# Kernel tuning notes

Hardware: AMD Instinct MI355X
Metric: run time of the kernel (lower is better)

## Reference

```python
import jax, jax.numpy as jnp
import numpy as np

N_NODES = 50000
N_REL = 3
N_EDGES = 500000
D_IN, D_HID, D_OUT = 128, 256, 128


def setup_inputs() -> dict:
    key = jax.random.key(0)
    ks = jax.random.split(key, 9)
    def w(k, shape, fan_in):
        return jax.random.normal(k, shape, dtype=jnp.float32) / np.sqrt(fan_in)
    return {
        "x": jax.random.normal(ks[0], (N_NODES, D_IN), dtype=jnp.float32),
        "src": jax.random.randint(ks[1], (N_REL, N_EDGES), 0, N_NODES, dtype=jnp.int32),
        "dst": jax.random.randint(ks[2], (N_REL, N_EDGES), 0, N_NODES, dtype=jnp.int32),
        "w_self1": w(ks[3], (N_REL, D_IN, D_HID), D_IN),
        "w_neigh1": w(ks[4], (N_REL, D_IN, D_HID), D_IN),
        "b1": jnp.zeros((N_REL, D_HID), dtype=jnp.float32),
        "w_self2": w(ks[5], (N_REL, D_HID, D_OUT), D_HID),
        "w_neigh2": w(ks[6], (N_REL, D_HID, D_OUT), D_HID),
        "b2": jnp.zeros((N_REL, D_OUT), dtype=jnp.float32),
    }


def _sage_hetero_layer(x, src, dst, w_self, w_neigh, b):
    """Multi-relation SAGEConv (mean agg); relation outputs summed (HeteroGraphConv default).
    x: [N, din]; src/dst: [R, E]; w_*: [R, din, dout]; b: [R, dout]."""
    n = x.shape[0]

    def per_rel(s, d, ws, wn, bb):
        gathered = jnp.take(x, s, axis=0)                      # [E, din] neighbor gather
        summed = jax.ops.segment_sum(gathered, d, num_segments=n)  # [N, din]
        deg = jax.ops.segment_sum(jnp.ones(s.shape, jnp.float32), d, num_segments=n)
        h_neigh = summed / jnp.maximum(deg, 1.0)[:, None]      # mean, 0 for isolated dst
        return x @ ws + h_neigh @ wn + bb                      # fc_self + fc_neigh + bias

    per_rel_out = jax.vmap(per_rel)(src, dst, w_self, w_neigh, b)  # [R, N, dout]
    return per_rel_out.sum(axis=0)


def reference(x, src, dst, w_self1, w_neigh1, b1, w_self2, w_neigh2, b2):
    h = _sage_hetero_layer(x, src, dst, w_self1, w_neigh1, b1)
    h = jax.nn.relu(h)  # SAGEConv activation in hidden layers
    out = _sage_hetero_layer(h, src, dst, w_self2, w_neigh2, b2)  # last layer: no activation
    return out
```

## Files before the change

kernel.cpp:

```cpp
#include <hip/hip_runtime.h>

#define NN 50000
#define NREL 3
#define NE 500000
#define DIN 128
#define DHID 256
#define DOUT 128

#define NBUK 98
#define CAP 8192
#define EPB 4096
#define NCHK ((NE + EPB - 1) / EPB)
#define PA_BLKS (NREL * NCHK)
#define F2B_BLKS 6250
#define ZROW ((uint)NN << 8)

typedef unsigned int uint;
typedef unsigned short ushort;
typedef __attribute__((ext_vector_type(8))) short bf16x8;
typedef __attribute__((ext_vector_type(4))) float f32x4;
typedef __attribute__((ext_vector_type(2))) float f32x2;

using gptr_t = const __attribute__((address_space(1))) unsigned int*;
using lptr_t = __attribute__((address_space(3))) unsigned int*;

__device__ __forceinline__ ushort f2bf(float f) {
    uint u = __float_as_uint(f);
    uint r = (u + 0x7fffu + ((u >> 16) & 1u)) >> 16;
    return (ushort)r;
}
__device__ __forceinline__ void acc2(f32x2& a, uint u) {
    f32x2 t;
    t.x = __uint_as_float(u << 16);
    t.y = __uint_as_float(u & 0xffff0000u);
    a += t;
}
__device__ __forceinline__ void acc16(f32x2* a, uint4 v) {
    acc2(a[0], v.x); acc2(a[1], v.y); acc2(a[2], v.z); acc2(a[3], v.w);
}

__global__ __launch_bounds__(256) void pass_a_prep(
    const int* __restrict__ src, const int* __restrict__ dst,
    int* __restrict__ bcursor, uint* __restrict__ pairs,
    const float* __restrict__ x, ushort* __restrict__ xb,
    const float* __restrict__ ws1, const float* __restrict__ wn1, ushort* __restrict__ Bt1,
    const float* __restrict__ ws2, const float* __restrict__ wn2, ushort* __restrict__ Bt2,
    const float* __restrict__ b1, float* __restrict__ bsum1,
    const float* __restrict__ b2, float* __restrict__ bsum2,
    ushort* __restrict__ agg0, ushort* __restrict__ agg1, ushort* __restrict__ agg2) {
    int blk = blockIdx.x, tid = threadIdx.x;
    if (blk < PA_BLKS) {
        int r = blk / NCHK;
        int chunk = blk % NCHK;
        int e0 = chunk * EPB;
        int nedge = min(EPB, NE - e0);
        const int* S = src + (size_t)r * NE + e0;
        const int* D = dst + (size_t)r * NE + e0;
        __shared__ int cnt[NBUK], base[NBUK], cur[NBUK];
        if (tid < NBUK) { cnt[tid] = 0; cur[tid] = 0; }
        __syncthreads();
        uint pk[16];
        int bk[16];
        bool val[16];
#pragma unroll
        for (int j = 0; j < 16; ++j) {
            int e = j * 256 + tid;
            val[j] = e < nedge;
            int d = val[j] ? D[e] : 0;
            int s = val[j] ? S[e] : 0;
            bk[j] = d >> 9;
            pk[j] = ((uint)s << 9) | (uint)(d & 511);
            if (val[j]) atomicAdd(&cnt[bk[j]], 1);
        }
        __syncthreads();
        if (tid < NBUK) base[tid] = atomicAdd(&bcursor[r * NBUK + tid], cnt[tid]);
        __syncthreads();
#pragma unroll
        for (int j = 0; j < 16; ++j) {
            if (val[j]) {
                int slot = base[bk[j]] + atomicAdd(&cur[bk[j]], 1);
                if (slot < CAP) pairs[(size_t)(r * NBUK + bk[j]) * CAP + slot] = pk[j];
            }
        }
        return;
    }
    blk -= PA_BLKS;
    if (blk < F2B_BLKS) {
        int t = blk * 256 + tid;
        float4 v = *(const float4*)(x + (size_t)t * 4);
        uint2 p;
        p.x = (uint)f2bf(v.x) | ((uint)f2bf(v.y) << 16);
        p.y = (uint)f2bf(v.z) | ((uint)f2bf(v.w) << 16);
        *(uint2*)(xb + (size_t)t * 4) = p;
    } else if (blk < F2B_BLKS + 512) {
        int t = (blk - F2B_BLKS) * 256 + tid;
        int n = t >> 9, k = t & 511;
        int b = k >> 7, kk = k & 127;
        float v;
        if (b == 0)
            v = ws1[kk * 256 + n] + ws1[128 * 256 + kk * 256 + n] + ws1[2 * 128 * 256 + kk * 256 + n];
        else
            v = wn1[(size_t)(b - 1) * 128 * 256 + kk * 256 + n];
        Bt1[t] = f2bf(v);
    } else if (blk < F2B_BLKS + 1024) {
        int t = (blk - F2B_BLKS - 512) * 256 + tid;
        int n = t >> 8, k = t & 255;
        int c = n >> 7, j = n & 127;
        float v;
        if (c == 0)
            v = ws2[k * 128 + j] + ws2[256 * 128 + k * 128 + j] + ws2[2 * 256 * 128 + k * 128 + j];
        else
            v = wn2[(size_t)(c - 1) * 256 * 128 + k * 128 + j];
        Bt2[t] = f2bf(v);
    } else {
        if (tid < DHID) bsum1[tid] = b1[tid] + b1[DHID + tid] + b1[2 * DHID + tid];
        if (tid < DOUT) bsum2[tid] = b2[tid] + b2[DOUT + tid] + b2[2 * DOUT + tid];
        if (tid >= 192 && tid < 256) {
            int b = (tid - 192) >> 4, i = tid & 15;
            ushort* row = (b == 0) ? xb : (b == 1) ? agg0 : (b == 2) ? agg1 : agg2;
            uint4 z = {0u, 0u, 0u, 0u};
            *(uint4*)(row + (size_t)NN * 128 + i * 8) = z;
        }
    }
}

__global__ __launch_bounds__(256) void pass_b(const uint* __restrict__ pairs,
                                              const int* __restrict__ bcnt,
                                              uint* __restrict__ srclist,
                                              int2* __restrict__ nd) {
    int blk = blockIdx.x;
    int b = blk % NBUK;
    int r = blk / NBUK;
    int node_base = b * 512;
    int count = min(bcnt[blk], CAP);
    int obase = blk * CAP;
    const uint* pp = pairs + (size_t)blk * CAP;
    __shared__ int hist[512];
    __shared__ int cur[512];
    __shared__ int sc[256];
    int tid = threadIdx.x;
    hist[tid] = 0;
    hist[tid + 256] = 0;
    __syncthreads();
    for (int i = tid; i < count; i += 256) atomicAdd(&hist[pp[i] & 511], 1);
    __syncthreads();
    int v0 = hist[2 * tid], v1 = hist[2 * tid + 1];
    int p0 = (v0 + 7) & ~7;
    int p1 = (v1 + 7) & ~7;
    int s = p0 + p1;
    sc[tid] = s;
    __syncthreads();
    for (int st = 1; st < 256; st <<= 1) {
        int t = (tid >= st) ? sc[tid - st] : 0;
        __syncthreads();
        sc[tid] += t;
        __syncthreads();
    }
    int excl = sc[tid] - s;
    int c0 = obase + excl;
    int c1 = c0 + p0;
    cur[2 * tid] = c0;
    cur[2 * tid + 1] = c1;
    int n0 = node_base + 2 * tid;
    if (n0 < NN)     nd[r * NN + n0]     = make_int2(v0, c0);
    if (n0 + 1 < NN) nd[r * NN + n0 + 1] = make_int2(v1, c1);
    __syncthreads();
    for (int i = tid; i < count; i += 256) {
        uint p = pp[i];
        int pos = atomicAdd(&cur[p & 511], 1);
        srclist[pos] = (p >> 1) & ~255u;
    }
    __syncthreads();
    for (int i = v0; i < p0; ++i) srclist[c0 + i] = ZROW;
    for (int i = v1; i < p1; ++i) srclist[c1 + i] = ZROW;
}

template <int PHASE>
__device__ __forceinline__ void gather_body(
    int node, int tid,
    const ushort* __restrict__ f0, const ushort* __restrict__ f1,
    const ushort* __restrict__ f2, const int2* __restrict__ nd,
    const uint* __restrict__ srclist,
    ushort* __restrict__ ob, float* __restrict__ of) {
    int lane = tid & 63;
    int g = lane >> 4;
    uint c16 = (uint)(lane & 15) * 16;
    const char* fp0 = (const char*)f0;
    const char* fp1 = (const char*)f1;
    const char* fp2 = (const char*)f2;

    int2 q0 = nd[node];
    int2 q1 = nd[NN + node];
    int2 q2 = nd[2 * NN + node];
    int d0 = q0.x, d1 = q1.x, d2 = q2.x;
    int pd0 = (d0 + 7) & ~7, pd1 = (d1 + 7) & ~7, pd2 = (d2 + 7) & ~7;
    uint sid0 = srclist[q0.y + lane];
    uint sid1 = srclist[q1.y + lane];
    uint sid2 = srclist[q2.y + lane];

    f32x2 a0[4], a1[4], a2[4];
#pragma unroll
    for (int k = 0; k < 4; ++k) { a0[k] = 0.f; a1[k] = 0.f; a2[k] = 0.f; }

    uint zoff = ZROW + c16;
    int pmax = max(max(pd0, pd1), pd2);
    int pm64 = min(pmax, 64);
    for (int j0 = 0; j0 < pm64; j0 += 8) {
        uint oA = (j0 < pd0) ? (__shfl(sid0, j0 + g) + c16) : zoff;
        uint oB = (j0 < pd0) ? (__shfl(sid0, j0 + 4 + g) + c16) : zoff;
        uint oC = (j0 < pd1) ? (__shfl(sid1, j0 + g) + c16) : zoff;
        uint oD = (j0 < pd1) ? (__shfl(sid1, j0 + 4 + g) + c16) : zoff;
        uint oE = (j0 < pd2) ? (__shfl(sid2, j0 + g) + c16) : zoff;
        uint oF = (j0 < pd2) ? (__shfl(sid2, j0 + 4 + g) + c16) : zoff;
        uint4 vA = *(const uint4*)(fp0 + oA);
        uint4 vB = *(const uint4*)(fp0 + oB);
        uint4 vC = *(const uint4*)(fp1 + oC);
        uint4 vD = *(const uint4*)(fp1 + oD);
        uint4 vE = *(const uint4*)(fp2 + oE);
        uint4 vF = *(const uint4*)(fp2 + oF);
        acc16(a0, vA); acc16(a0, vB);
        acc16(a1, vC); acc16(a1, vD);
        acc16(a2, vE); acc16(a2, vF);
    }
    if (pmax > 64) {
        for (int i0 = 64; i0 < pd0; i0 += 64) {
            uint sl = srclist[q0.y + i0 + lane];
            int lim = min(pd0 - i0, 64);
            for (int j0 = 0; j0 < lim; j0 += 8) {
                uint u1 = __shfl(sl, j0 + g) + c16, u2 = __shfl(sl, j0 + 4 + g) + c16;
                acc16(a0, *(const uint4*)(fp0 + u1));
                acc16(a0, *(const uint4*)(fp0 + u2));
            }
        }
        for (int i0 = 64; i0 < pd1; i0 += 64) {
            uint sl = srclist[q1.y + i0 + lane];
            int lim = min(pd1 - i0, 64);
            for (int j0 = 0; j0 < lim; j0 += 8) {
                uint u1 = __shfl(sl, j0 + g) + c16, u2 = __shfl(sl, j0 + 4 + g) + c16;
                acc16(a1, *(const uint4*)(fp1 + u1));
                acc16(a1, *(const uint4*)(fp1 + u2));
            }
        }
        for (int i0 = 64; i0 < pd2; i0 += 64) {
            uint sl = srclist[q2.y + i0 + lane];
            int lim = min(pd2 - i0, 64);
            for (int j0 = 0; j0 < lim; j0 += 8) {
                uint u1 = __shfl(sl, j0 + g) + c16, u2 = __shfl(sl, j0 + 4 + g) + c16;
                acc16(a2, *(const uint4*)(fp2 + u1));
                acc16(a2, *(const uint4*)(fp2 + u2));
            }
        }
    }

#pragma unroll
    for (int k = 0; k < 4; ++k) {
        a0[k].x += __shfl_xor(a0[k].x, 16); a0[k].y += __shfl_xor(a0[k].y, 16);
        a0[k].x += __shfl_xor(a0[k].x, 32); a0[k].y += __shfl_xor(a0[k].y, 32);
        a1[k].x += __shfl_xor(a1[k].x, 16); a1[k].y += __shfl_xor(a1[k].y, 16);
        a1[k].x += __shfl_xor(a1[k].x, 32); a1[k].y += __shfl_xor(a1[k].y, 32);
        a2[k].x += __shfl_xor(a2[k].x, 16); a2[k].y += __shfl_xor(a2[k].y, 16);
        a2[k].x += __shfl_xor(a2[k].x, 32); a2[k].y += __shfl_xor(a2[k].y, 32);
    }
    float inv0 = 1.f / fmaxf((float)d0, 1.f);
    float inv1 = 1.f / fmaxf((float)d1, 1.f);
    float inv2 = 1.f / fmaxf((float)d2, 1.f);
    if (PHASE == 0) {
        if (g == 0) {
            size_t base = (size_t)node * 128 + (c16 >> 1);
            size_t rstride = (size_t)(NN + 1) * DIN;
            uint4 pk;
            pk.x = (uint)f2bf(a0[0].x * inv0) | ((uint)f2bf(a0[0].y * inv0) << 16);
            pk.y = (uint)f2bf(a0[1].x * inv0) | ((uint)f2bf(a0[1].y * inv0) << 16);
            pk.z = (uint)f2bf(a0[2].x * inv0) | ((uint)f2bf(a0[2].y * inv0) << 16);
            pk.w = (uint)f2bf(a0[3].x * inv0) | ((uint)f2bf(a0[3].y * inv0) << 16);
            *(uint4*)(ob + base) = pk;
            pk.x = (uint)f2bf(a1[0].x * inv1) | ((uint)f2bf(a1[0].y * inv1) << 16);
            pk.y = (uint)f2bf(a1[1].x * inv1) | ((uint)f2bf(a1[1].y * inv1) << 16);
            pk.z = (uint)f2bf(a1[2].x * inv1) | ((uint)f2bf(a1[2].y * inv1) << 16);
            pk.w = (uint)f2bf(a1[3].x * inv1) | ((uint)f2bf(a1[3].y * inv1) << 16);
            *(uint4*)(ob + rstride + base) = pk;
            pk.x = (uint)f2bf(a2[0].x * inv2) | ((uint)f2bf(a2[0].y * inv2) << 16);
            pk.y = (uint)f2bf(a2[1].x * inv2) | ((uint)f2bf(a2[1].y * inv2) << 16);
            pk.z = (uint)f2bf(a2[2].x * inv2) | ((uint)f2bf(a2[2].y * inv2) << 16);
            pk.w = (uint)f2bf(a2[3].x * inv2) | ((uint)f2bf(a2[3].y * inv2) << 16);
            *(uint4*)(ob + 2 * rstride + base) = pk;
        }
    } else {
        if (g == 0) {
            float* po = of + (size_t)node * 128 + (c16 >> 1);
            float4 a = *(float4*)po;
            float4 b = *(float4*)(po + 4);
            a.x += a0[0].x * inv0 + a1[0].x * inv1 + a2[0].x * inv2;
            a.y += a0[0].y * inv0 + a1[0].y * inv1 + a2[0].y * inv2;
            a.z += a0[1].x * inv0 + a1[1].x * inv1 + a2[1].x * inv2;
            a.w += a0[1].y * inv0 + a1[1].y * inv1 + a2[1].y * inv2;
            b.x += a0[2].x * inv0 + a1[2].x * inv1 + a2[2].x * inv2;
            b.y += a0[2].y * inv0 + a1[2].y * inv1 + a2[2].y * inv2;
            b.z += a0[3].x * inv0 + a1[3].x * inv1 + a2[3].x * inv2;
            b.w += a0[3].y * inv0 + a1[3].y * inv1 + a2[3].y * inv2;
            *(float4*)po = a;
            *(float4*)(po + 4) = b;
        }
    }
}

__global__ __launch_bounds__(256) void gather_p0(
    const ushort* __restrict__ xb, const int2* __restrict__ nd,
    const uint* __restrict__ srclist, ushort* __restrict__ aggb) {
    int node = blockIdx.x * 4 + (threadIdx.x >> 6);
    if (node < NN)
        gather_body<0>(node, threadIdx.x, xb, xb, xb, nd, srclist, aggb, nullptr);
}

__global__ __launch_bounds__(256) void gather_p1(
    const ushort* __restrict__ f0, const ushort* __restrict__ f1,
    const ushort* __restrict__ f2, const int2* __restrict__ nd,
    const uint* __restrict__ srclist, float* __restrict__ of) {
    int node = blockIdx.x * 4 + (threadIdx.x >> 6);
    if (node < NN)
        gather_body<1>(node, threadIdx.x, f0, f1, f2, nd, srclist, nullptr, of);
}

template <int LAYER>
__global__ __launch_bounds__(512) void gemm_mfma(
    const ushort* __restrict__ A0, const ushort* __restrict__ A1,
    const ushort* __restrict__ A2, const ushort* __restrict__ A3,
    const ushort* __restrict__ Bt, const float* __restrict__ bias,
    ushort* __restrict__ HO, float* __restrict__ CO,
    ushort* __restrict__ Y1, ushort* __restrict__ Y2, ushort* __restrict__ Y3) {
    constexpr int KTOT = (LAYER == 1) ? 512 : 256;
    constexpr int ASTRIDE = (LAYER == 1) ? 128 : 256;
    constexpr int NT = KTOT / 32;
    __shared__ __align__(16) ushort As[2][128 * 32];
    __shared__ __align__(16) ushort Bs[2][256 * 32];

    const int tid = threadIdx.x, lane = tid & 63, w = tid >> 6;
    const int wr = w >> 2, wc = w & 3;
    const int bm = blockIdx.x * 128;
    const int bn = blockIdx.y * 256;
    const int srow = tid >> 2;
    const int schunk = (tid & 3) * 8;

    f32x4 acc[4][4];
#pragma unroll
    for (int m = 0; m < 4; ++m)
#pragma unroll
        for (int n = 0; n < 4; ++n) acc[m][n] = (f32x4){0.f, 0.f, 0.f, 0.f};

    auto stage = [&](int t, int buf) {
        int k0 = t * 32;
        const ushort* Ab = A0;
        int koff = k0;
        if (LAYER == 1) {
            int b = k0 >> 7;
            Ab = (b == 0) ? A0 : (b == 1) ? A1 : (b == 2) ? A2 : A3;
            koff = k0 & 127;
        }
        const ushort* srcA = Ab + (size_t)(bm + srow) * ASTRIDE + koff + schunk;
        __builtin_amdgcn_global_load_lds((gptr_t)srcA, (lptr_t)(&As[buf][w * 512]), 16, 0, 0);
#pragma unroll
        for (int i = 0; i < 2; ++i) {
            const ushort* srcB = Bt + (size_t)(bn + i * 128 + srow) * KTOT + k0 + schunk;
            __builtin_amdgcn_global_load_lds((gptr_t)srcB, (lptr_t)(&Bs[buf][i * 4096 + w * 512]), 16, 0, 0);
        }
    };

    stage(0, 0);
    const int r = lane & 15, g = lane >> 4;
    for (int t = 0; t < NT; ++t) {
        int cur = t & 1;
        if (t + 1 < NT) {
            stage(t + 1, cur ^ 1);
            asm volatile("s_waitcnt vmcnt(3)" ::: "memory");
        } else {
            asm volatile("s_waitcnt vmcnt(0)" ::: "memory");
        }
        __builtin_amdgcn_s_barrier();
        asm volatile("" ::: "memory");
        bf16x8 af[4], bg[4];
#pragma unroll
        for (int m = 0; m < 4; ++m)
            af[m] = *(const bf16x8*)&As[cur][(wr * 64 + m * 16 + r) * 32 + g * 8];
#pragma unroll
        for (int n = 0; n < 4; ++n)
            bg[n] = *(const bf16x8*)&Bs[cur][(wc * 64 + n * 16 + r) * 32 + g * 8];
#pragma unroll
        for (int m = 0; m < 4; ++m)
#pragma unroll
            for (int n = 0; n < 4; ++n)
                acc[m][n] = __builtin_amdgcn_mfma_f32_16x16x32_bf16(af[m], bg[n], acc[m][n], 0, 0, 0);
        asm volatile("" ::: "memory");
        __builtin_amdgcn_s_barrier();
    }

    if (LAYER == 1) {
#pragma unroll
        for (int m = 0; m < 4; ++m)
#pragma unroll
            for (int v = 0; v < 4; ++v) {
                int gm = bm + wr * 64 + m * 16 + g * 4 + v;
                if (gm >= NN) continue;
#pragma unroll
                for (int n = 0; n < 4; ++n) {
                    int gn = wc * 64 + n * 16 + r;
                    float f = acc[m][n][v] + bias[gn];
                    f = fmaxf(f, 0.f);
                    HO[(size_t)gm * 256 + gn] = f2bf(f);
                }
            }
    } else {
        int buf = (bn >> 7) + (wc >> 1);
        ushort* Y = (buf == 1) ? Y1 : (buf == 2) ? Y2 : Y3;
#pragma unroll
        for (int m = 0; m < 4; ++m)
#pragma unroll
            for (int v = 0; v < 4; ++v) {
                int gm = bm + wr * 64 + m * 16 + g * 4 + v;
                if (gm >= NN) continue;
#pragma unroll
                for (int n = 0; n < 4; ++n) {
                    int col = (wc & 1) * 64 + n * 16 + r;
                    if (buf == 0)
                        CO[(size_t)gm * 128 + col] = acc[m][n][v] + bias[col];
                    else
                        Y[(size_t)gm * 128 + col] = f2bf(acc[m][n][v]);
                }
            }
    }
}

extern "C" void kernel_launch(void* const* d_in, const int* in_sizes, int n_in,
                              void* d_out, int out_size, void* d_ws, size_t ws_size,
                              hipStream_t stream) {
    const float* x        = (const float*)d_in[0];
    const int*   src      = (const int*)d_in[1];
    const int*   dst      = (const int*)d_in[2];
    const float* w_self1  = (const float*)d_in[3];
    const float* w_neigh1 = (const float*)d_in[4];
    const float* b1       = (const float*)d_in[5];
    const float* w_self2  = (const float*)d_in[6];
    const float* w_neigh2 = (const float*)d_in[7];
    const float* b2       = (const float*)d_in[8];
    float* out = (float*)d_out;

    char* ws = (char*)d_ws;
    size_t off = 0;
    auto alloc = [&](size_t bytes) {
        char* p = ws + off;
        off += (bytes + 255) & ~(size_t)255;
        return p;
    };
    const size_t NROW = NN + 1;
    int*    bcursor = (int*)alloc(NREL * NBUK * 4);
    int2*   nd      = (int2*)alloc((size_t)NREL * NN * 8);
    uint*   srclist = (uint*)alloc(((size_t)NREL * NBUK * CAP + 256) * 4);
    float*  bsum1   = (float*)alloc(DHID * 4);
    float*  bsum2   = (float*)alloc(DOUT * 4);
    ushort* Bt1     = (ushort*)alloc((size_t)DHID * 512 * 2);
    ushort* Bt2     = (ushort*)alloc((size_t)512 * DHID * 2);
    ushort* xb      = (ushort*)alloc(NROW * DIN * 2);
    ushort* aggb    = (ushort*)alloc((size_t)NREL * NROW * DIN * 2);
    ushort* Hb      = (ushort*)alloc((size_t)NN * DHID * 2);
    (void)alloc(65536);
    uint* pairs = (uint*)Hb;
    ushort* agg0 = aggb;
    ushort* agg1 = aggb + NROW * DIN;
    ushort* agg2 = aggb + 2 * NROW * DIN;

    hipMemsetAsync(bcursor, 0, NREL * NBUK * 4, stream);
    pass_a_prep<<<PA_BLKS + F2B_BLKS + 1024 + 1, 256, 0, stream>>>(
        src, dst, bcursor, pairs,
        x, xb, w_self1, w_neigh1, Bt1, w_self2, w_neigh2, Bt2,
        b1, bsum1, b2, bsum2, agg0, agg1, agg2);
    pass_b<<<NREL * NBUK, 256, 0, stream>>>(pairs, bcursor, srclist, nd);

    int ggrid = (NN + 3) / 4;

    gather_p0<<<ggrid, 256, 0, stream>>>(xb, nd, srclist, aggb);
    {
        dim3 grid((NN + 127) / 128, 1);
        gemm_mfma<1><<<grid, 512, 0, stream>>>(
            xb, agg0, agg1, agg2, Bt1, bsum1, Hb, nullptr, nullptr, nullptr, nullptr);
    }
    {
        dim3 grid((NN + 127) / 128, 2);
        gemm_mfma<2><<<grid, 512, 0, stream>>>(
            Hb, nullptr, nullptr, nullptr, Bt2, bsum2,
            nullptr, out, agg0, agg1, agg2);
    }
    gather_p1<<<ggrid, 256, 0, stream>>>(agg0, agg1, agg2, nd, srclist, out);
}
```

Baseline: 224.8 us.

## Slice bf16 feature buffers into 32-column planes for cache-local gathers

Feature matrices (xb, agg, Y) are stored as four column slices of 32 bf16 values per node, so each gather block touches only a 64-byte slice per neighbor and the per-slice working set fits better in L2. Both gather kernels process one slice per block, gather_p1 is split into three launches (one per relation), and nontemporal loads and stores are used for index and output traffic. The GEMMs read and write the sliced layout. The cost is four times as many gather blocks, repeated index reads for each slice, and three extra read-modify-write passes over the output in layer 2.

```diff
diff --git a/kernel.cpp b/kernel.cpp
--- a/kernel.cpp
+++ b/kernel.cpp
@@ -13,13 +13,18 @@
 #define NCHK ((NE + EPB - 1) / EPB)
 #define PA_BLKS (NREL * NCHK)
 #define F2B_BLKS 6250
-#define ZROW ((uint)NN << 8)
+#define NROW (NN + 1)
+#define SS ((size_t)NROW * 32)
+#define ZROW ((uint)NN << 6)
 
 typedef unsigned int uint;
 typedef unsigned short ushort;
+typedef unsigned long long u64;
 typedef __attribute__((ext_vector_type(8))) short bf16x8;
 typedef __attribute__((ext_vector_type(4))) float f32x4;
 typedef __attribute__((ext_vector_type(2))) float f32x2;
+typedef __attribute__((ext_vector_type(4))) uint u32x4;
+typedef __attribute__((ext_vector_type(2))) uint u32x2;
 
 using gptr_t = const __attribute__((address_space(1))) unsigned int*;
 using lptr_t = __attribute__((address_space(3))) unsigned int*;
@@ -35,7 +40,7 @@
     t.y = __uint_as_float(u & 0xffff0000u);
     a += t;
 }
-__device__ __forceinline__ void acc16(f32x2* a, uint4 v) {
+__device__ __forceinline__ void acc16(f32x2* a, u32x4 v) {
     acc2(a[0], v.x); acc2(a[1], v.y); acc2(a[2], v.z); acc2(a[3], v.w);
 }
 
@@ -47,7 +52,7 @@
     const float* __restrict__ ws2, const float* __restrict__ wn2, ushort* __restrict__ Bt2,
     const float* __restrict__ b1, float* __restrict__ bsum1,
     const float* __restrict__ b2, float* __restrict__ bsum2,
-    ushort* __restrict__ agg0, ushort* __restrict__ agg1, ushort* __restrict__ agg2) {
+    ushort* __restrict__ aggb) {
     int blk = blockIdx.x, tid = threadIdx.x;
     if (blk < PA_BLKS) {
         int r = blk / NCHK;
@@ -87,11 +92,15 @@
     blk -= PA_BLKS;
     if (blk < F2B_BLKS) {
         int t = blk * 256 + tid;
-        float4 v = *(const float4*)(x + (size_t)t * 4);
+        int sl = t / (NN * 8);
+        int rem = t - sl * (NN * 8);
+        int node = rem >> 3;
+        int dq = (rem & 7) * 4;
+        float4 v = *(const float4*)(x + (size_t)node * 128 + sl * 32 + dq);
         uint2 p;
         p.x = (uint)f2bf(v.x) | ((uint)f2bf(v.y) << 16);
         p.y = (uint)f2bf(v.z) | ((uint)f2bf(v.w) << 16);
-        *(uint2*)(xb + (size_t)t * 4) = p;
+        *(uint2*)(xb + (size_t)sl * SS + (size_t)node * 32 + dq) = p;
     } else if (blk < F2B_BLKS + 512) {
         int t = (blk - F2B_BLKS) * 256 + tid;
         int n = t >> 9, k = t & 511;
@@ -115,11 +124,11 @@
     } else {
         if (tid < DHID) bsum1[tid] = b1[tid] + b1[DHID + tid] + b1[2 * DHID + tid];
         if (tid < DOUT) bsum2[tid] = b2[tid] + b2[DOUT + tid] + b2[2 * DOUT + tid];
-        if (tid >= 192 && tid < 256) {
-            int b = (tid - 192) >> 4, i = tid & 15;
-            ushort* row = (b == 0) ? xb : (b == 1) ? agg0 : (b == 2) ? agg1 : agg2;
+        if (tid >= 192) {
+            int p = (tid - 192) >> 2, c = tid & 3;
+            ushort* base = (p < 4) ? (xb + (size_t)p * SS) : (aggb + (size_t)(p - 4) * SS);
             uint4 z = {0u, 0u, 0u, 0u};
-            *(uint4*)(row + (size_t)NN * 128 + i * 8) = z;
+            *(uint4*)(base + (size_t)NN * 32 + c * 8) = z;
         }
     }
 }
@@ -168,157 +177,180 @@
     for (int i = tid; i < count; i += 256) {
         uint p = pp[i];
         int pos = atomicAdd(&cur[p & 511], 1);
-        srclist[pos] = (p >> 1) & ~255u;
+        srclist[pos] = (p >> 3) & ~63u;
     }
     __syncthreads();
     for (int i = v0; i < p0; ++i) srclist[c0 + i] = ZROW;
     for (int i = v1; i < p1; ++i) srclist[c1 + i] = ZROW;
 }
 
-template <int PHASE>
-__device__ __forceinline__ void gather_body(
-    int node, int tid,
-    const ushort* __restrict__ f0, const ushort* __restrict__ f1,
-    const ushort* __restrict__ f2, const int2* __restrict__ nd,
-    const uint* __restrict__ srclist,
-    ushort* __restrict__ ob, float* __restrict__ of) {
-    int lane = tid & 63;
-    int g = lane >> 4;
-    uint c16 = (uint)(lane & 15) * 16;
-    const char* fp0 = (const char*)f0;
-    const char* fp1 = (const char*)f1;
-    const char* fp2 = (const char*)f2;
-
-    int2 q0 = nd[node];
-    int2 q1 = nd[NN + node];
-    int2 q2 = nd[2 * NN + node];
-    int d0 = q0.x, d1 = q1.x, d2 = q2.x;
-    int pd0 = (d0 + 7) & ~7, pd1 = (d1 + 7) & ~7, pd2 = (d2 + 7) & ~7;
-    uint sid0 = srclist[q0.y + lane];
-    uint sid1 = srclist[q1.y + lane];
-    uint sid2 = srclist[q2.y + lane];
-
-    f32x2 a0[4], a1[4], a2[4];
-#pragma unroll
-    for (int k = 0; k < 4; ++k) { a0[k] = 0.f; a1[k] = 0.f; a2[k] = 0.f; }
-
-    uint zoff = ZROW + c16;
-    int pmax = max(max(pd0, pd1), pd2);
-    int pm64 = min(pmax, 64);
-    for (int j0 = 0; j0 < pm64; j0 += 8) {
-        uint oA = (j0 < pd0) ? (__shfl(sid0, j0 + g) + c16) : zoff;
-        uint oB = (j0 < pd0) ? (__shfl(sid0, j0 + 4 + g) + c16) : zoff;
-        uint oC = (j0 < pd1) ? (__shfl(sid1, j0 + g) + c16) : zoff;
-        uint oD = (j0 < pd1) ? (__shfl(sid1, j0 + 4 + g) + c16) : zoff;
-        uint oE = (j0 < pd2) ? (__shfl(sid2, j0 + g) + c16) : zoff;
-        uint oF = (j0 < pd2) ? (__shfl(sid2, j0 + 4 + g) + c16) : zoff;
-        uint4 vA = *(const uint4*)(fp0 + oA);
-        uint4 vB = *(const uint4*)(fp0 + oB);
-        uint4 vC = *(const uint4*)(fp1 + oC);
-        uint4 vD = *(const uint4*)(fp1 + oD);
-        uint4 vE = *(const uint4*)(fp2 + oE);
-        uint4 vF = *(const uint4*)(fp2 + oF);
-        acc16(a0, vA); acc16(a0, vB);
-        acc16(a1, vC); acc16(a1, vD);
-        acc16(a2, vE); acc16(a2, vF);
-    }
-    if (pmax > 64) {
-        for (int i0 = 64; i0 < pd0; i0 += 64) {
-            uint sl = srclist[q0.y + i0 + lane];
-            int lim = min(pd0 - i0, 64);
-            for (int j0 = 0; j0 < lim; j0 += 8) {
-                uint u1 = __shfl(sl, j0 + g) + c16, u2 = __shfl(sl, j0 + 4 + g) + c16;
-                acc16(a0, *(const uint4*)(fp0 + u1));
-                acc16(a0, *(const uint4*)(fp0 + u2));
-            }
-        }
-        for (int i0 = 64; i0 < pd1; i0 += 64) {
-            uint sl = srclist[q1.y + i0 + lane];
-            int lim = min(pd1 - i0, 64);
-            for (int j0 = 0; j0 < lim; j0 += 8) {
-                uint u1 = __shfl(sl, j0 + g) + c16, u2 = __shfl(sl, j0 + 4 + g) + c16;
-                acc16(a1, *(const uint4*)(fp1 + u1));
-                acc16(a1, *(const uint4*)(fp1 + u2));
-            }
-        }
-        for (int i0 = 64; i0 < pd2; i0 += 64) {
-            uint sl = srclist[q2.y + i0 + lane];
-            int lim = min(pd2 - i0, 64);
-            for (int j0 = 0; j0 < lim; j0 += 8) {
-                uint u1 = __shfl(sl, j0 + g) + c16, u2 = __shfl(sl, j0 + 4 + g) + c16;
-                acc16(a2, *(const uint4*)(fp2 + u1));
-                acc16(a2, *(const uint4*)(fp2 + u2));
-            }
-        }
-    }
-
-#pragma unroll
-    for (int k = 0; k < 4; ++k) {
-        a0[k].x += __shfl_xor(a0[k].x, 16); a0[k].y += __shfl_xor(a0[k].y, 16);
-        a0[k].x += __shfl_xor(a0[k].x, 32); a0[k].y += __shfl_xor(a0[k].y, 32);
-        a1[k].x += __shfl_xor(a1[k].x, 16); a1[k].y += __shfl_xor(a1[k].y, 16);
-        a1[k].x += __shfl_xor(a1[k].x, 32); a1[k].y += __shfl_xor(a1[k].y, 32);
-        a2[k].x += __shfl_xor(a2[k].x, 16); a2[k].y += __shfl_xor(a2[k].y, 16);
-        a2[k].x += __shfl_xor(a2[k].x, 32); a2[k].y += __shfl_xor(a2[k].y, 32);
-    }
-    float inv0 = 1.f / fmaxf((float)d0, 1.f);
-    float inv1 = 1.f / fmaxf((float)d1, 1.f);
-    float inv2 = 1.f / fmaxf((float)d2, 1.f);
-    if (PHASE == 0) {
-        if (g == 0) {
-            size_t base = (size_t)node * 128 + (c16 >> 1);
-            size_t rstride = (size_t)(NN + 1) * DIN;
-            uint4 pk;
-            pk.x = (uint)f2bf(a0[0].x * inv0) | ((uint)f2bf(a0[0].y * inv0) << 16);
-            pk.y = (uint)f2bf(a0[1].x * inv0) | ((uint)f2bf(a0[1].y * inv0) << 16);
-            pk.z = (uint)f2bf(a0[2].x * inv0) | ((uint)f2bf(a0[2].y * inv0) << 16);
-            pk.w = (uint)f2bf(a0[3].x * inv0) | ((uint)f2bf(a0[3].y * inv0) << 16);
-            *(uint4*)(ob + base) = pk;
-            pk.x = (uint)f2bf(a1[0].x * inv1) | ((uint)f2bf(a1[0].y * inv1) << 16);
-            pk.y = (uint)f2bf(a1[1].x * inv1) | ((uint)f2bf(a1[1].y * inv1) << 16);
-            pk.z = (uint)f2bf(a1[2].x * inv1) | ((uint)f2bf(a1[2].y * inv1) << 16);
-            pk.w = (uint)f2bf(a1[3].x * inv1) | ((uint)f2bf(a1[3].y * inv1) << 16);
-            *(uint4*)(ob + rstride + base) = pk;
-            pk.x = (uint)f2bf(a2[0].x * inv2) | ((uint)f2bf(a2[0].y * inv2) << 16);
-            pk.y = (uint)f2bf(a2[1].x * inv2) | ((uint)f2bf(a2[1].y * inv2) << 16);
-            pk.z = (uint)f2bf(a2[2].x * inv2) | ((uint)f2bf(a2[2].y * inv2) << 16);
-            pk.w = (uint)f2bf(a2[3].x * inv2) | ((uint)f2bf(a2[3].y * inv2) << 16);
-            *(uint4*)(ob + 2 * rstride + base) = pk;
-        }
-    } else {
-        if (g == 0) {
-            float* po = of + (size_t)node * 128 + (c16 >> 1);
-            float4 a = *(float4*)po;
-            float4 b = *(float4*)(po + 4);
-            a.x += a0[0].x * inv0 + a1[0].x * inv1 + a2[0].x * inv2;
-            a.y += a0[0].y * inv0 + a1[0].y * inv1 + a2[0].y * inv2;
-            a.z += a0[1].x * inv0 + a1[1].x * inv1 + a2[1].x * inv2;
-            a.w += a0[1].y * inv0 + a1[1].y * inv1 + a2[1].y * inv2;
-            b.x += a0[2].x * inv0 + a1[2].x * inv1 + a2[2].x * inv2;
-            b.y += a0[2].y * inv0 + a1[2].y * inv1 + a2[2].y * inv2;
-            b.z += a0[3].x * inv0 + a1[3].x * inv1 + a2[3].x * inv2;
-            b.w += a0[3].y * inv0 + a1[3].y * inv1 + a2[3].y * inv2;
-            *(float4*)po = a;
-            *(float4*)(po + 4) = b;
-        }
-    }
-}
-
 __global__ __launch_bounds__(256) void gather_p0(
     const ushort* __restrict__ xb, const int2* __restrict__ nd,
     const uint* __restrict__ srclist, ushort* __restrict__ aggb) {
-    int node = blockIdx.x * 4 + (threadIdx.x >> 6);
-    if (node < NN)
-        gather_body<0>(node, threadIdx.x, xb, xb, xb, nd, srclist, aggb, nullptr);
+    int sl = blockIdx.x & 3;
+    int node = (blockIdx.x >> 2) * 4 + (threadIdx.x >> 6);
+    if (node >= NN) return;
+    int lane = threadIdx.x & 63;
+    int e = lane >> 2;
+    uint c16 = (uint)(lane & 3) * 16;
+    const char* fp = (const char*)(xb + (size_t)sl * SS);
+
+    const u64* ndp = (const u64*)nd;
+    u64 n0 = __builtin_nontemporal_load(ndp + node);
+    u64 n1 = __builtin_nontemporal_load(ndp + NN + node);
+    u64 n2 = __builtin_nontemporal_load(ndp + 2 * NN + node);
+    int d0 = (int)(uint)n0, b0 = (int)(n0 >> 32);
+    int d1 = (int)(uint)n1, b1 = (int)(n1 >> 32);
+    int d2 = (int)(uint)n2, b2 = (int)(n2 >> 32);
+    int pd0 = (d0 + 7) & ~7, pd1 = (d1 + 7) & ~7, pd2 = (d2 + 7) & ~7;
+    uint sid0 = __builtin_nontemporal_load(srclist + b0 + lane);
+    uint sid1 = __builtin_nontemporal_load(srclist + b1 + lane);
+    uint sid2 = __builtin_nontemporal_load(srclist + b2 + lane);
+
+    f32x2 a0[4], a1[4], a2[4];
+#pragma unroll
+    for (int k = 0; k < 4; ++k) { a0[k] = 0.f; a1[k] = 0.f; a2[k] = 0.f; }
+
+    uint zoff = ZROW + c16;
+    int pmax = max(max(pd0, pd1), pd2);
+    int pm = min(pmax, 64);
+    for (int j0 = 0; j0 < pm; j0 += 16) {
+        int i = j0 + e;
+        uint oA = (i < pd0) ? (__shfl(sid0, i) + c16) : zoff;
+        uint oB = (i < pd1) ? (__shfl(sid1, i) + c16) : zoff;
+        uint oC = (i < pd2) ? (__shfl(sid2, i) + c16) : zoff;
+        u32x4 vA = *(const u32x4*)(fp + oA);
+        u32x4 vB = *(const u32x4*)(fp + oB);
+        u32x4 vC = *(const u32x4*)(fp + oC);
+        acc16(a0, vA);
+        acc16(a1, vB);
+        acc16(a2, vC);
+    }
+    if (pmax > 64) {
+        for (int i0 = 64; i0 < pd0; i0 += 64) {
+            uint s2 = __builtin_nontemporal_load(srclist + b0 + i0 + lane);
+            int lim = min(pd0 - i0, 64);
+            for (int j0 = 0; j0 < lim; j0 += 16) {
+                int i = j0 + e;
+                uint o = (i < lim) ? (__shfl(s2, i) + c16) : zoff;
+                acc16(a0, *(const u32x4*)(fp + o));
+            }
+        }
+        for (int i0 = 64; i0 < pd1; i0 += 64) {
+            uint s2 = __builtin_nontemporal_load(srclist + b1 + i0 + lane);
+            int lim = min(pd1 - i0, 64);
+            for (int j0 = 0; j0 < lim; j0 += 16) {
+                int i = j0 + e;
+                uint o = (i < lim) ? (__shfl(s2, i) + c16) : zoff;
+                acc16(a1, *(const u32x4*)(fp + o));
+            }
+        }
+        for (int i0 = 64; i0 < pd2; i0 += 64) {
+            uint s2 = __builtin_nontemporal_load(srclist + b2 + i0 + lane);
+            int lim = min(pd2 - i0, 64);
+            for (int j0 = 0; j0 < lim; j0 += 16) {
+                int i = j0 + e;
+                uint o = (i < lim) ? (__shfl(s2, i) + c16) : zoff;
+                acc16(a2, *(const u32x4*)(fp + o));
+            }
+        }
+    }
+
+#pragma unroll
+    for (int k = 0; k < 4; ++k) {
+#pragma unroll
+        for (int m = 4; m <= 32; m <<= 1) {
+            a0[k].x += __shfl_xor(a0[k].x, m); a0[k].y += __shfl_xor(a0[k].y, m);
+            a1[k].x += __shfl_xor(a1[k].x, m); a1[k].y += __shfl_xor(a1[k].y, m);
+            a2[k].x += __shfl_xor(a2[k].x, m); a2[k].y += __shfl_xor(a2[k].y, m);
+        }
+    }
+    if (e == 0) {
+        float inv0 = 1.f / fmaxf((float)d0, 1.f);
+        float inv1 = 1.f / fmaxf((float)d1, 1.f);
+        float inv2 = 1.f / fmaxf((float)d2, 1.f);
+        size_t base = (size_t)sl * SS + (size_t)node * 32 + (lane & 3) * 8;
+        u32x4 pk;
+        pk.x = (uint)f2bf(a0[0].x * inv0) | ((uint)f2bf(a0[0].y * inv0) << 16);
+        pk.y = (uint)f2bf(a0[1].x * inv0) | ((uint)f2bf(a0[1].y * inv0) << 16);
+        pk.z = (uint)f2bf(a0[2].x * inv0) | ((uint)f2bf(a0[2].y * inv0) << 16);
+        pk.w = (uint)f2bf(a0[3].x * inv0) | ((uint)f2bf(a0[3].y * inv0) << 16);
+        __builtin_nontemporal_store(pk, (u32x4*)(aggb + base));
+        pk.x = (uint)f2bf(a1[0].x * inv1) | ((uint)f2bf(a1[0].y * inv1) << 16);
+        pk.y = (uint)f2bf(a1[1].x * inv1) | ((uint)f2bf(a1[1].y * inv1) << 16);
+        pk.z = (uint)f2bf(a1[2].x * inv1) | ((uint)f2bf(a1[2].y * inv1) << 16);
+        pk.w = (uint)f2bf(a1[3].x * inv1) | ((uint)f2bf(a1[3].y * inv1) << 16);
+        __builtin_nontemporal_store(pk, (u32x4*)(aggb + 4 * SS + base));
+        pk.x = (uint)f2bf(a2[0].x * inv2) | ((uint)f2bf(a2[0].y * inv2) << 16);
+        pk.y = (uint)f2bf(a2[1].x * inv2) | ((uint)f2bf(a2[1].y * inv2) << 16);
+        pk.z = (uint)f2bf(a2[2].x * inv2) | ((uint)f2bf(a2[2].y * inv2) << 16);
+        pk.w = (uint)f2bf(a2[3].x * inv2) | ((uint)f2bf(a2[3].y * inv2) << 16);
+        __builtin_nontemporal_store(pk, (u32x4*)(aggb + 8 * SS + base));
+    }
 }
 
 __global__ __launch_bounds__(256) void gather_p1(
-    const ushort* __restrict__ f0, const ushort* __restrict__ f1,
-    const ushort* __restrict__ f2, const int2* __restrict__ nd,
-    const uint* __restrict__ srclist, float* __restrict__ of) {
-    int node = blockIdx.x * 4 + (threadIdx.x >> 6);
-    if (node < NN)
-        gather_body<1>(node, threadIdx.x, f0, f1, f2, nd, srclist, nullptr, of);
+    const ushort* __restrict__ Y, const int2* __restrict__ nd_r,
+    const uint* __restrict__ srclist, float* __restrict__ out) {
+    int sl = blockIdx.x & 3;
+    int node = (blockIdx.x >> 2) * 4 + (threadIdx.x >> 6);
+    if (node >= NN) return;
+    int lane = threadIdx.x & 63;
+    int e = lane >> 2;
+    uint c16 = (uint)(lane & 3) * 16;
+    const char* fp = (const char*)(Y + (size_t)sl * SS);
+
+    u64 n0 = __builtin_nontemporal_load((const u64*)nd_r + node);
+    int d = (int)(uint)n0, beg = (int)(n0 >> 32);
+    int pd = (d + 7) & ~7;
+    uint sid = __builtin_nontemporal_load(srclist + beg + lane);
+
+    f32x2 a[4];
+#pragma unroll
+    for (int k = 0; k < 4; ++k) a[k] = 0.f;
+
+    uint zoff = ZROW + c16;
+    int pm = min(pd, 64);
+    for (int j0 = 0; j0 < pm; j0 += 32) {
+        int i1 = j0 + e, i2 = j0 + 16 + e;
+        uint o1 = (i1 < pd) ? (__shfl(sid, i1) + c16) : zoff;
+        uint o2 = (i2 < pd) ? (__shfl(sid, i2) + c16) : zoff;
+        u32x4 v1 = *(const u32x4*)(fp + o1);
+        u32x4 v2 = *(const u32x4*)(fp + o2);
+        acc16(a, v1);
+        acc16(a, v2);
+    }
+    if (pd > 64) {
+        for (int i0 = 64; i0 < pd; i0 += 64) {
+            uint s2 = __builtin_nontemporal_load(srclist + beg + i0 + lane);
+            int lim = min(pd - i0, 64);
+            for (int j0 = 0; j0 < lim; j0 += 16) {
+                int i = j0 + e;
+                uint o = (i < lim) ? (__shfl(s2, i) + c16) : zoff;
+                acc16(a, *(const u32x4*)(fp + o));
+            }
+        }
+    }
+#pragma unroll
+    for (int k = 0; k < 4; ++k) {
+#pragma unroll
+        for (int m = 4; m <= 32; m <<= 1) {
+            a[k].x += __shfl_xor(a[k].x, m);
+            a[k].y += __shfl_xor(a[k].y, m);
+        }
+    }
+    if (e == 0) {
+        float inv = 1.f / fmaxf((float)d, 1.f);
+        f32x4* po = (f32x4*)(out + (size_t)node * 128 + sl * 32 + (lane & 3) * 8);
+        f32x4 v0 = __builtin_nontemporal_load(po);
+        f32x4 v1 = __builtin_nontemporal_load(po + 1);
+        v0.x += a[0].x * inv; v0.y += a[0].y * inv;
+        v0.z += a[1].x * inv; v0.w += a[1].y * inv;
+        v1.x += a[2].x * inv; v1.y += a[2].y * inv;
+        v1.z += a[3].x * inv; v1.w += a[3].y * inv;
+        __builtin_nontemporal_store(v0, po);
+        __builtin_nontemporal_store(v1, po + 1);
+    }
 }
 
 template <int LAYER>
@@ -329,7 +361,6 @@
     ushort* __restrict__ HO, float* __restrict__ CO,
     ushort* __restrict__ Y1, ushort* __restrict__ Y2, ushort* __restrict__ Y3) {
     constexpr int KTOT = (LAYER == 1) ? 512 : 256;
-    constexpr int ASTRIDE = (LAYER == 1) ? 128 : 256;
     constexpr int NT = KTOT / 32;
     __shared__ __align__(16) ushort As[2][128 * 32];
     __shared__ __align__(16) ushort Bs[2][256 * 32];
@@ -349,14 +380,14 @@
 
     auto stage = [&](int t, int buf) {
         int k0 = t * 32;
-        const ushort* Ab = A0;
-        int koff = k0;
+        const ushort* srcA;
         if (LAYER == 1) {
             int b = k0 >> 7;
-            Ab = (b == 0) ? A0 : (b == 1) ? A1 : (b == 2) ? A2 : A3;
-            koff = k0 & 127;
-        }
-        const ushort* srcA = Ab + (size_t)(bm + srow) * ASTRIDE + koff + schunk;
+            const ushort* Ab = (b == 0) ? A0 : (b == 1) ? A1 : (b == 2) ? A2 : A3;
+            srcA = Ab + (size_t)((k0 >> 5) & 3) * SS + (size_t)(bm + srow) * 32 + schunk;
+        } else {
+            srcA = A0 + (size_t)(bm + srow) * 256 + k0 + schunk;
+        }
         __builtin_amdgcn_global_load_lds((gptr_t)srcA, (lptr_t)(&As[buf][w * 512]), 16, 0, 0);
 #pragma unroll
         for (int i = 0; i < 2; ++i) {
@@ -423,7 +454,7 @@
                     if (buf == 0)
                         CO[(size_t)gm * 128 + col] = acc[m][n][v] + bias[col];
                     else
-                        Y[(size_t)gm * 128 + col] = f2bf(acc[m][n][v]);
+                        Y[(size_t)(col >> 5) * SS + (size_t)gm * 32 + (col & 31)] = f2bf(acc[m][n][v]);
                 }
             }
     }
@@ -450,7 +481,6 @@
         off += (bytes + 255) & ~(size_t)255;
         return p;
     };
-    const size_t NROW = NN + 1;
     int*    bcursor = (int*)alloc(NREL * NBUK * 4);
     int2*   nd      = (int2*)alloc((size_t)NREL * NN * 8);
     uint*   srclist = (uint*)alloc(((size_t)NREL * NBUK * CAP + 256) * 4);
@@ -458,25 +488,25 @@
     float*  bsum2   = (float*)alloc(DOUT * 4);
     ushort* Bt1     = (ushort*)alloc((size_t)DHID * 512 * 2);
     ushort* Bt2     = (ushort*)alloc((size_t)512 * DHID * 2);
-    ushort* xb      = (ushort*)alloc(NROW * DIN * 2);
-    ushort* aggb    = (ushort*)alloc((size_t)NREL * NROW * DIN * 2);
+    ushort* xb      = (ushort*)alloc(4 * SS * 2);
+    ushort* aggb    = (ushort*)alloc(12 * SS * 2);
     ushort* Hb      = (ushort*)alloc((size_t)NN * DHID * 2);
     (void)alloc(65536);
     uint* pairs = (uint*)Hb;
     ushort* agg0 = aggb;
-    ushort* agg1 = aggb + NROW * DIN;
-    ushort* agg2 = aggb + 2 * NROW * DIN;
+    ushort* agg1 = aggb + 4 * SS;
+    ushort* agg2 = aggb + 8 * SS;
 
     hipMemsetAsync(bcursor, 0, NREL * NBUK * 4, stream);
     pass_a_prep<<<PA_BLKS + F2B_BLKS + 1024 + 1, 256, 0, stream>>>(
         src, dst, bcursor, pairs,
         x, xb, w_self1, w_neigh1, Bt1, w_self2, w_neigh2, Bt2,
-        b1, bsum1, b2, bsum2, agg0, agg1, agg2);
+        b1, bsum1, b2, bsum2, aggb);
     pass_b<<<NREL * NBUK, 256, 0, stream>>>(pairs, bcursor, srclist, nd);
 
-    int ggrid = (NN + 3) / 4;
-
-    gather_p0<<<ggrid, 256, 0, stream>>>(xb, nd, srclist, aggb);
+    int sgrid = 4 * ((NN + 3) / 4);
+
+    gather_p0<<<sgrid, 256, 0, stream>>>(xb, nd, srclist, aggb);
     {
         dim3 grid((NN + 127) / 128, 1);
         gemm_mfma<1><<<grid, 512, 0, stream>>>(
@@ -488,5 +518,7 @@
             Hb, nullptr, nullptr, nullptr, Bt2, bsum2,
             nullptr, out, agg0, agg1, agg2);
     }
-    gather_p1<<<ggrid, 256, 0, stream>>>(agg0, agg1, agg2, nd, srclist, out);
-}
+    gather_p1<<<sgrid, 256, 0, stream>>>(agg0, nd, srclist, out);
+    gather_p1<<<sgrid, 256, 0, stream>>>(agg1, nd + (size_t)NN, srclist, out);
+    gather_p1<<<sgrid, 256, 0, stream>>>(agg2, nd + (size_t)2 * NN, srclist, out);
+}
```

New measurement: 558.8 us. 2.49x slower.
